# Optimization experiments

Measured on AMD Instinct MI355X. Metric: run time of the kernel, lower is better.

The kernel has to match this reference:

```python
import jax, jax.numpy as jnp
import numpy as np

TOP_K = 2
AUX_COEFF = 0.01

def setup_inputs() -> dict:
    key = jax.random.key(0)
    k1, k2, k3, k4 = jax.random.split(key, 4)
    B, T, d, E = 4, 1024, 1024, 8
    x = jax.random.normal(k1, (B, T, d), dtype=jnp.float32)
    w_gate = jax.random.normal(k2, (d, E), dtype=jnp.float32) * 0.02
    w1 = jax.random.normal(k3, (E, d, 4 * d), dtype=jnp.float32) * 0.02
    w2 = jax.random.normal(k4, (E, 4 * d, d), dtype=jnp.float32) * 0.02
    return {"x": x, "w_gate": w_gate, "w1": w1, "w2": w2}

def reference(x, w_gate, w1, w2):
    B, T, d = x.shape
    E = w_gate.shape[1]
    N = B * T
    xf = x.reshape(N, d)

    # Router: softmax over experts, top-k, renormalize
    logits = xf @ w_gate                      # [N, E]
    probs = jax.nn.softmax(logits, axis=-1)   # [N, E]
    topk_p, topk_i = jax.lax.top_k(probs, TOP_K)
    topk_p = topk_p / topk_p.sum(axis=-1, keepdims=True)

    # Combine weights: scatter top-k probs into [N, E] (equiv. to masked scatter-add loop)
    comb = jnp.zeros((N, E), dtype=x.dtype).at[
        jnp.arange(N)[:, None], topk_i].add(topk_p)

    # Grouped expert MLP (dense over experts, weighted combine)
    h = jnp.einsum('nd,edf->enf', xf, w1)     # [E, N, 4d]
    h = jax.nn.gelu(h, approximate=False)     # exact erf GELU like nn.GELU
    y = jnp.einsum('enf,efd->end', h, w2)     # [E, N, d]
    out = jnp.einsum('ne,end->nd', comb, y).reshape(B, T, d)

    # Load-balancing aux loss (training branch)
    counts = jnp.zeros((E,), dtype=x.dtype).at[topk_i.reshape(-1)].add(1.0)
    f = counts / (N * TOP_K)
    p = probs.mean(axis=0)
    aux_loss = AUX_COEFF * E * jnp.sum(f * p)
    return out, aux_loss
```

## Files before the change

### kernel.cpp

```cpp
#include <hip/hip_runtime.h>
#include <cmath>

#define N_TOK 4096
#define DDIM 1024
#define FDIM 4096
#define NEXP 8
#define MAXT 72
#define MAXROWS (MAXT * 128)

typedef __attribute__((ext_vector_type(4))) float f32x4;
typedef __attribute__((ext_vector_type(8))) __bf16 bf16x8;
typedef __attribute__((ext_vector_type(4))) unsigned short us4;
typedef __attribute__((ext_vector_type(8))) unsigned short us8;

__device__ __forceinline__ unsigned short f2bf(float f) {
  unsigned u = __builtin_bit_cast(unsigned, f);
  u += 0x7FFFu + ((u >> 16) & 1u);
  return (unsigned short)(u >> 16);
}

__device__ __forceinline__ void gload16(const void* g, void* l) {
  __builtin_amdgcn_global_load_lds(
      (const __attribute__((address_space(1))) unsigned int*)g,
      (__attribute__((address_space(3))) unsigned int*)l, 16, 0, 0);
}

__global__ __launch_bounds__(64) void router_kernel(
    const float* __restrict__ x, const float* __restrict__ wg,
    float* __restrict__ probs, int* __restrict__ eids, float* __restrict__ ewts) {
  int n = blockIdx.x;
  int t = threadIdx.x;
  const float* xr = x + (size_t)n * DDIM;
  float acc[8] = {0, 0, 0, 0, 0, 0, 0, 0};
  for (int k = t; k < DDIM; k += 64) {
    float xv = xr[k];
    const float* wr = wg + k * 8;
#pragma unroll
    for (int e = 0; e < 8; e++) acc[e] = fmaf(xv, wr[e], acc[e]);
  }
#pragma unroll
  for (int off = 32; off > 0; off >>= 1) {
#pragma unroll
    for (int e = 0; e < 8; e++) acc[e] += __shfl_xor(acc[e], off, 64);
  }
  if (t == 0) {
    float mx = acc[0];
#pragma unroll
    for (int e = 1; e < 8; e++) mx = fmaxf(mx, acc[e]);
    float p[8], s = 0.f;
#pragma unroll
    for (int e = 0; e < 8; e++) { p[e] = expf(acc[e] - mx); s += p[e]; }
    float inv = 1.f / s;
#pragma unroll
    for (int e = 0; e < 8; e++) { p[e] *= inv; probs[n * 8 + e] = p[e]; }
    int i0 = 0;
#pragma unroll
    for (int e = 1; e < 8; e++) if (p[e] > p[i0]) i0 = e;
    int i1 = (i0 == 0) ? 1 : 0;
#pragma unroll
    for (int e = 0; e < 8; e++) if (e != i0 && p[e] > p[i1]) i1 = e;
    float sw = p[i0] + p[i1];
    eids[n * 2] = i0; eids[n * 2 + 1] = i1;
    ewts[n * 2] = p[i0] / sw; ewts[n * 2 + 1] = p[i1] / sw;
  }
}

__global__ __launch_bounds__(256) void plan_kernel(
    const float* __restrict__ probs, const int* __restrict__ eids,
    float* __restrict__ aux_out, int* __restrict__ meta) {
  __shared__ float pl[256][8];
  __shared__ int cl[256][8];
  __shared__ float ps2[8];
  __shared__ int cn2[8];
  int t = threadIdx.x;
  float pa[8] = {0, 0, 0, 0, 0, 0, 0, 0};
  int ca[8] = {0, 0, 0, 0, 0, 0, 0, 0};
  for (int n = t; n < N_TOK; n += 256) {
#pragma unroll
    for (int e = 0; e < 8; e++) pa[e] += probs[n * 8 + e];
    ca[eids[n * 2]]++; ca[eids[n * 2 + 1]]++;
  }
#pragma unroll
  for (int e = 0; e < 8; e++) { pl[t][e] = pa[e]; cl[t][e] = ca[e]; }
  __syncthreads();
  if (t < 8) {
    float s = 0; int c = 0;
    for (int i = 0; i < 256; i++) { s += pl[i][t]; c += cl[i][t]; }
    ps2[t] = s; cn2[t] = c;
  }
  __syncthreads();
  if (t == 0) {
    int tb = 0; float aux = 0.f;
    for (int e = 0; e < 8; e++) {
      int c = cn2[e];
      meta[e] = c; meta[8 + e] = 0; meta[16 + e] = tb;
      int tiles = (c + 127) >> 7;
      for (int i = 0; i < tiles; i++) meta[24 + tb + i] = e;
      tb += tiles;
      aux += ((float)c / (float)(N_TOK * 2)) * (ps2[e] / (float)N_TOK);
    }
    meta[96] = tb;
    *aux_out = 0.01f * 8.f * aux;
  }
}

__global__ __launch_bounds__(256) void scatter_kernel(
    const int* __restrict__ eids, const float* __restrict__ ewts,
    int* __restrict__ meta, int* __restrict__ perm, float* __restrict__ wgt) {
  int n = blockIdx.x * 256 + threadIdx.x;
  if (n >= N_TOK) return;
#pragma unroll
  for (int s = 0; s < 2; s++) {
    int e = eids[n * 2 + s];
    int pos = atomicAdd(&meta[8 + e], 1);
    int row = (meta[16 + e] << 7) + pos;
    perm[row] = n;
    wgt[row] = ewts[n * 2 + s];
  }
}

__global__ __launch_bounds__(256) void convert_x_kernel(
    const float* __restrict__ x, unsigned short* __restrict__ xb) {
  int i = blockIdx.x * 256 + threadIdx.x;
  f32x4 v = ((const f32x4*)x)[i];
  us4 o = {f2bf(v[0]), f2bf(v[1]), f2bf(v[2]), f2bf(v[3])};
  ((us4*)xb)[i] = o;
}

__global__ __launch_bounds__(256) void transpose_conv(
    const float* __restrict__ src, unsigned short* __restrict__ dst, int R, int C) {
  __shared__ unsigned short tile[64 * 64];
  size_t eoff = (size_t)blockIdx.z * (size_t)R * (size_t)C;
  src += eoff; dst += eoff;
  int c0 = blockIdx.x << 6, r0 = blockIdx.y << 6;
  int t = threadIdx.x;
  int rl = (t >> 4) << 2;
  int cl = (t & 15) << 2;
  f32x4 v[4];
#pragma unroll
  for (int i = 0; i < 4; i++)
    v[i] = *(const f32x4*)(src + (size_t)(r0 + rl + i) * C + c0 + cl);
#pragma unroll
  for (int u = 0; u < 4; u++) {
    int c = cl + u;
    us4 o = {f2bf(v[0][u]), f2bf(v[1][u]), f2bf(v[2][u]), f2bf(v[3][u])};
    unsigned byteoff = (unsigned)c * 128 + ((((unsigned)(rl >> 3)) ^ (unsigned)(c & 7)) << 4) + (unsigned)(rl & 7) * 2;
    *(us4*)((char*)tile + byteoff) = o;
  }
  __syncthreads();
#pragma unroll
  for (int p = 0; p < 2; p++) {
    int id = t + p * 256;
    int c = id >> 3, q = id & 7;
    unsigned byteoff = (unsigned)c * 128 + (((unsigned)q ^ (unsigned)(c & 7)) << 4);
    us8 val = *(const us8*)((const char*)tile + byteoff);
    *(us8*)(dst + (size_t)(c0 + c) * R + r0 + q * 8) = val;
  }
}

template <int K, bool GATHER, int MODE>
__global__ __launch_bounds__(256, 2) void gemm_kernel(
    const unsigned short* __restrict__ A,
    const unsigned short* __restrict__ Bt,
    unsigned short* __restrict__ Hout,
    float* __restrict__ Out,
    const int* __restrict__ perm, const float* __restrict__ wgt,
    const int* __restrict__ tileExpert, const int* __restrict__ totalTiles,
    int NB) {
  __shared__ unsigned short ldsA[128 * 64];
  __shared__ unsigned short ldsB[128 * 64];
  int tile = blockIdx.x;
  if (tile >= *totalTiles) return;
  int e = tileExpert[tile];
  int m0 = tile << 7;
  int n0 = blockIdx.y << 7;
  const unsigned short* Bbase = Bt + ((size_t)e * NB + n0) * K;
  int t = threadIdx.x;
  int wave = t >> 6, lane = t & 63;
  int g = lane >> 4, ln = lane & 15;
  int wm = wave >> 1, wn = wave & 1;

  const unsigned short* srcA[4];
  const unsigned short* srcB[4];
#pragma unroll
  for (int i = 0; i < 4; i++) {
    int c = wave * 256 + i * 64 + lane;
    int r = c >> 3, kc = c & 7;
    int rowA = GATHER ? perm[m0 + r] : (m0 + r);
    srcA[i] = A + (size_t)rowA * K + ((kc ^ (r & 7)) << 3);
    srcB[i] = Bbase + (size_t)r * K + ((kc ^ (r & 7)) << 3);
  }

  f32x4 acc[4][4];
#pragma unroll
  for (int a = 0; a < 4; a++)
#pragma unroll
    for (int b = 0; b < 4; b++) acc[a][b] = (f32x4){0.f, 0.f, 0.f, 0.f};

  for (int k0 = 0; k0 < K; k0 += 64) {
#pragma unroll
    for (int i = 0; i < 4; i++) {
      int cb = wave * 256 + i * 64;
      gload16(srcA[i] + k0, &ldsA[cb * 8]);
      gload16(srcB[i] + k0, &ldsB[cb * 8]);
    }
    __syncthreads();
#pragma unroll
    for (int ks = 0; ks < 2; ks++) {
      bf16x8 af[4], bfr[4];
      int q = ks * 4 + g;
#pragma unroll
      for (int mf = 0; mf < 4; mf++) {
        int m = wm * 64 + mf * 16 + ln;
        af[mf] = *(const bf16x8*)((const char*)ldsA + m * 128 + ((q ^ (m & 7)) << 4));
      }
#pragma unroll
      for (int nf = 0; nf < 4; nf++) {
        int n = wn * 64 + nf * 16 + ln;
        bfr[nf] = *(const bf16x8*)((const char*)ldsB + n * 128 + ((q ^ (n & 7)) << 4));
      }
#pragma unroll
      for (int mf = 0; mf < 4; mf++)
#pragma unroll
        for (int nf = 0; nf < 4; nf++)
          acc[mf][nf] = __builtin_amdgcn_mfma_f32_16x16x32_bf16(af[mf], bfr[nf], acc[mf][nf], 0, 0, 0);
    }
    __syncthreads();
  }

  if (MODE == 1) {
#pragma unroll
    for (int mf = 0; mf < 4; mf++) {
#pragma unroll
      for (int r = 0; r < 4; r++) {
        int row = m0 + wm * 64 + mf * 16 + g * 4 + r;
        unsigned short* hp = Hout + (size_t)row * NB + n0 + wn * 64 + ln;
#pragma unroll
        for (int nf = 0; nf < 4; nf++) {
          float v = acc[mf][nf][r];
          v = 0.5f * v * (1.f + erff(v * 0.70710678118654752f));
          hp[nf * 16] = f2bf(v);
        }
      }
    }
  } else {
#pragma unroll
    for (int mf = 0; mf < 4; mf++) {
#pragma unroll
      for (int r = 0; r < 4; r++) {
        int prow = m0 + wm * 64 + mf * 16 + g * 4 + r;
        int token = perm[prow];
        float wv = wgt[prow];
        float* op = Out + (size_t)token * NB + n0 + wn * 64 + ln;
#pragma unroll
        for (int nf = 0; nf < 4; nf++)
          atomicAdd(op + nf * 16, wv * acc[mf][nf][r]);
      }
    }
  }
}

extern "C" void kernel_launch(void* const* d_in, const int* in_sizes, int n_in,
                              void* d_out, int out_size, void* d_ws, size_t ws_size,
                              hipStream_t stream) {
  const float* x = (const float*)d_in[0];
  const float* wgate = (const float*)d_in[1];
  const float* w1 = (const float*)d_in[2];
  const float* w2 = (const float*)d_in[3];
  float* out = (float*)d_out;

  char* w = (char*)d_ws;
  float* probs = (float*)w;                 w += (size_t)N_TOK * 8 * 4;
  int* eids = (int*)w;                      w += (size_t)N_TOK * 2 * 4;
  float* ewts = (float*)w;                  w += (size_t)N_TOK * 2 * 4;
  int* meta = (int*)w;                      w += 512;
  int* perm = (int*)w;                      w += (size_t)MAXROWS * 4;
  float* pwgt = (float*)w;                  w += (size_t)MAXROWS * 4;
  unsigned short* xb = (unsigned short*)w;  w += (size_t)N_TOK * DDIM * 2;
  unsigned short* w1t = (unsigned short*)w; w += (size_t)NEXP * DDIM * FDIM * 2;
  unsigned short* w2t = (unsigned short*)w; w += (size_t)NEXP * DDIM * FDIM * 2;
  unsigned short* h = (unsigned short*)w;   w += (size_t)MAXROWS * FDIM * 2;

  hipMemsetAsync(d_out, 0, (size_t)out_size * 4, stream);
  hipMemsetAsync(perm, 0, (size_t)MAXROWS * 8, stream);

  router_kernel<<<N_TOK, 64, 0, stream>>>(x, wgate, probs, eids, ewts);
  plan_kernel<<<1, 256, 0, stream>>>(probs, eids, out + 4194304, meta);
  scatter_kernel<<<16, 256, 0, stream>>>(eids, ewts, meta, perm, pwgt);
  convert_x_kernel<<<4096, 256, 0, stream>>>(x, xb);
  transpose_conv<<<dim3(64, 16, 8), 256, 0, stream>>>(w1, w1t, DDIM, FDIM);
  transpose_conv<<<dim3(16, 64, 8), 256, 0, stream>>>(w2, w2t, FDIM, DDIM);
  gemm_kernel<DDIM, true, 1><<<dim3(MAXT, 32), 256, 0, stream>>>(
      xb, w1t, h, nullptr, perm, pwgt, meta + 24, meta + 96, FDIM);
  gemm_kernel<FDIM, false, 2><<<dim3(MAXT, 8), 256, 0, stream>>>(
      h, w2t, nullptr, out, perm, pwgt, meta + 24, meta + 96, DDIM);
}
```

Before: 468.2 us.

## Add XCD-aware grouped tile rasterization and split-K for the down-projection GEMM

Both expert GEMMs now use a flat 1D grid. Block IDs are remapped so that consecutive logical tiles land on the same XCD, and tiles are walked in 8x8 groups of M-tiles by N-panels so blocks that share A rows and B panels run close together and reuse L2. The second GEMM (K=4096) is split into two K-slices, doubling the number of workgroups to fill more CUs; it relies on the epilogue accumulating partial results into the zeroed output. The min-occupancy hint in launch_bounds is dropped, which may change register allocation.

Result: slower. 516.8 us (+10.4%).

```diff
diff --git a/kernel.cpp b/kernel.cpp
--- a/kernel.cpp
+++ b/kernel.cpp
@@ -23,6 +23,12 @@
   __builtin_amdgcn_global_load_lds(
       (const __attribute__((address_space(1))) unsigned int*)g,
       (__attribute__((address_space(3))) unsigned int*)l, 16, 0, 0);
+}
+
+__device__ __forceinline__ int xcd_remap(int h, int nwg) {
+  int q = nwg >> 3, r = nwg & 7;
+  int xcd = h & 7, o = h >> 3;
+  return (xcd < r ? xcd * (q + 1) : r * (q + 1) + (xcd - r) * q) + o;
 }
 
 __global__ __launch_bounds__(64) void router_kernel(
@@ -158,8 +164,8 @@
   }
 }
 
-template <int K, bool GATHER, int MODE>
-__global__ __launch_bounds__(256, 2) void gemm_kernel(
+template <int K, int KSLICES, int NPANELS, bool GATHER, int MODE>
+__global__ __launch_bounds__(256) void gemm_kernel(
     const unsigned short* __restrict__ A,
     const unsigned short* __restrict__ Bt,
     unsigned short* __restrict__ Hout,
@@ -167,13 +173,24 @@
     const int* __restrict__ perm, const float* __restrict__ wgt,
     const int* __restrict__ tileExpert, const int* __restrict__ totalTiles,
     int NB) {
+  constexpr int NWG = MAXT * NPANELS * KSLICES;
+  constexpr int KB = K / KSLICES;
   __shared__ unsigned short ldsA[128 * 64];
   __shared__ unsigned short ldsB[128 * 64];
-  int tile = blockIdx.x;
-  if (tile >= *totalTiles) return;
-  int e = tileExpert[tile];
-  int m0 = tile << 7;
-  int n0 = blockIdx.y << 7;
+
+  int L = xcd_remap(blockIdx.x, NWG);
+  int group = L >> 6, wi = L & 63;
+  int gm = group % (MAXT / 8), gcol = group / (MAXT / 8);
+  int mt = gm * 8 + (wi & 7);
+  int nc = gcol * 8 + (wi >> 3);
+  int nt = nc % NPANELS;
+  int ks = nc / NPANELS;
+
+  if (mt >= *totalTiles) return;
+  int e = tileExpert[mt];
+  int m0 = mt << 7;
+  int n0 = nt << 7;
+  int k0b = ks * KB;
   const unsigned short* Bbase = Bt + ((size_t)e * NB + n0) * K;
   int t = threadIdx.x;
   int wave = t >> 6, lane = t & 63;
@@ -187,8 +204,8 @@
     int c = wave * 256 + i * 64 + lane;
     int r = c >> 3, kc = c & 7;
     int rowA = GATHER ? perm[m0 + r] : (m0 + r);
-    srcA[i] = A + (size_t)rowA * K + ((kc ^ (r & 7)) << 3);
-    srcB[i] = Bbase + (size_t)r * K + ((kc ^ (r & 7)) << 3);
+    srcA[i] = A + (size_t)rowA * K + k0b + ((kc ^ (r & 7)) << 3);
+    srcB[i] = Bbase + (size_t)r * K + k0b + ((kc ^ (r & 7)) << 3);
   }
 
   f32x4 acc[4][4];
@@ -197,7 +214,7 @@
 #pragma unroll
     for (int b = 0; b < 4; b++) acc[a][b] = (f32x4){0.f, 0.f, 0.f, 0.f};
 
-  for (int k0 = 0; k0 < K; k0 += 64) {
+  for (int k0 = 0; k0 < KB; k0 += 64) {
 #pragma unroll
     for (int i = 0; i < 4; i++) {
       int cb = wave * 256 + i * 64;
@@ -206,9 +223,9 @@
     }
     __syncthreads();
 #pragma unroll
-    for (int ks = 0; ks < 2; ks++) {
+    for (int kss = 0; kss < 2; kss++) {
       bf16x8 af[4], bfr[4];
-      int q = ks * 4 + g;
+      int q = kss * 4 + g;
 #pragma unroll
       for (int mf = 0; mf < 4; mf++) {
         int m = wm * 64 + mf * 16 + ln;
@@ -290,8 +307,8 @@
   convert_x_kernel<<<4096, 256, 0, stream>>>(x, xb);
   transpose_conv<<<dim3(64, 16, 8), 256, 0, stream>>>(w1, w1t, DDIM, FDIM);
   transpose_conv<<<dim3(16, 64, 8), 256, 0, stream>>>(w2, w2t, FDIM, DDIM);
-  gemm_kernel<DDIM, true, 1><<<dim3(MAXT, 32), 256, 0, stream>>>(
+  gemm_kernel<DDIM, 1, 32, true, 1><<<MAXT * 32, 256, 0, stream>>>(
       xb, w1t, h, nullptr, perm, pwgt, meta + 24, meta + 96, FDIM);
-  gemm_kernel<FDIM, false, 2><<<dim3(MAXT, 8), 256, 0, stream>>>(
+  gemm_kernel<FDIM, 2, 8, false, 2><<<MAXT * 16, 256, 0, stream>>>(
       h, w2t, nullptr, out, perm, pwgt, meta + 24, meta + 96, DDIM);
 }
```

## Replace atomic scatter-add in down-projection with scratch store plus combine kernel

Applied to the files above, without the earlier changes.

The second GEMM now writes plain fp32 rows into a scratch buffer that reuses the w1t workspace, which is no longer needed by then, instead of doing weighted atomicAdd into the output. A new combine kernel gathers each token's two expert rows through an inverse permutation and applies the routing weights. This removes float atomics and the output memset, at the cost of an extra round trip through scratch memory and one more launch. The padding rows in the scratch buffer get written but are never read.

New measurement: 401.9 us. 14.2% less time.

```diff
diff --git a/kernel.cpp b/kernel.cpp
--- a/kernel.cpp
+++ b/kernel.cpp
@@ -105,8 +105,8 @@
 }
 
 __global__ __launch_bounds__(256) void scatter_kernel(
-    const int* __restrict__ eids, const float* __restrict__ ewts,
-    int* __restrict__ meta, int* __restrict__ perm, float* __restrict__ wgt) {
+    const int* __restrict__ eids, int* __restrict__ meta,
+    int* __restrict__ perm, int* __restrict__ inv) {
   int n = blockIdx.x * 256 + threadIdx.x;
   if (n >= N_TOK) return;
 #pragma unroll
@@ -115,7 +115,7 @@
     int pos = atomicAdd(&meta[8 + e], 1);
     int row = (meta[16 + e] << 7) + pos;
     perm[row] = n;
-    wgt[row] = ewts[n * 2 + s];
+    inv[n * 2 + s] = row;
   }
 }
 
@@ -164,7 +164,7 @@
     const unsigned short* __restrict__ Bt,
     unsigned short* __restrict__ Hout,
     float* __restrict__ Out,
-    const int* __restrict__ perm, const float* __restrict__ wgt,
+    const int* __restrict__ perm,
     const int* __restrict__ tileExpert, const int* __restrict__ totalTiles,
     int NB) {
   __shared__ unsigned short ldsA[128 * 64];
@@ -248,16 +248,27 @@
     for (int mf = 0; mf < 4; mf++) {
 #pragma unroll
       for (int r = 0; r < 4; r++) {
-        int prow = m0 + wm * 64 + mf * 16 + g * 4 + r;
-        int token = perm[prow];
-        float wv = wgt[prow];
-        float* op = Out + (size_t)token * NB + n0 + wn * 64 + ln;
-#pragma unroll
-        for (int nf = 0; nf < 4; nf++)
-          atomicAdd(op + nf * 16, wv * acc[mf][nf][r]);
+        int row = m0 + wm * 64 + mf * 16 + g * 4 + r;
+        float* yp = Out + (size_t)row * NB + n0 + wn * 64 + ln;
+#pragma unroll
+        for (int nf = 0; nf < 4; nf++) yp[nf * 16] = acc[mf][nf][r];
       }
     }
   }
+}
+
+__global__ __launch_bounds__(256) void combine_kernel(
+    const float* __restrict__ yscr, const int* __restrict__ inv,
+    const float* __restrict__ ewts, float* __restrict__ out) {
+  int n = blockIdx.x, t = threadIdx.x;
+  int r0 = inv[n * 2], r1 = inv[n * 2 + 1];
+  float w0 = ewts[n * 2], w1 = ewts[n * 2 + 1];
+  f32x4 a = *(const f32x4*)(yscr + (size_t)r0 * DDIM + t * 4);
+  f32x4 b = *(const f32x4*)(yscr + (size_t)r1 * DDIM + t * 4);
+  f32x4 o;
+#pragma unroll
+  for (int j = 0; j < 4; j++) o[j] = w0 * a[j] + w1 * b[j];
+  *(f32x4*)(out + (size_t)n * DDIM + t * 4) = o;
 }
 
 extern "C" void kernel_launch(void* const* d_in, const int* in_sizes, int n_in,
@@ -275,23 +286,24 @@
   float* ewts = (float*)w;                  w += (size_t)N_TOK * 2 * 4;
   int* meta = (int*)w;                      w += 512;
   int* perm = (int*)w;                      w += (size_t)MAXROWS * 4;
-  float* pwgt = (float*)w;                  w += (size_t)MAXROWS * 4;
+  int* inv = (int*)w;                       w += (size_t)N_TOK * 2 * 4;
   unsigned short* xb = (unsigned short*)w;  w += (size_t)N_TOK * DDIM * 2;
   unsigned short* w1t = (unsigned short*)w; w += (size_t)NEXP * DDIM * FDIM * 2;
   unsigned short* w2t = (unsigned short*)w; w += (size_t)NEXP * DDIM * FDIM * 2;
   unsigned short* h = (unsigned short*)w;   w += (size_t)MAXROWS * FDIM * 2;
-
-  hipMemsetAsync(d_out, 0, (size_t)out_size * 4, stream);
-  hipMemsetAsync(perm, 0, (size_t)MAXROWS * 8, stream);
+  float* yscr = (float*)w1t;
+
+  hipMemsetAsync(perm, 0, (size_t)MAXROWS * 4, stream);
 
   router_kernel<<<N_TOK, 64, 0, stream>>>(x, wgate, probs, eids, ewts);
   plan_kernel<<<1, 256, 0, stream>>>(probs, eids, out + 4194304, meta);
-  scatter_kernel<<<16, 256, 0, stream>>>(eids, ewts, meta, perm, pwgt);
+  scatter_kernel<<<16, 256, 0, stream>>>(eids, meta, perm, inv);
   convert_x_kernel<<<4096, 256, 0, stream>>>(x, xb);
   transpose_conv<<<dim3(64, 16, 8), 256, 0, stream>>>(w1, w1t, DDIM, FDIM);
   transpose_conv<<<dim3(16, 64, 8), 256, 0, stream>>>(w2, w2t, FDIM, DDIM);
   gemm_kernel<DDIM, true, 1><<<dim3(MAXT, 32), 256, 0, stream>>>(
-      xb, w1t, h, nullptr, perm, pwgt, meta + 24, meta + 96, FDIM);
+      xb, w1t, h, nullptr, perm, meta + 24, meta + 96, FDIM);
   gemm_kernel<FDIM, false, 2><<<dim3(MAXT, 8), 256, 0, stream>>>(
-      h, w2t, nullptr, out, perm, pwgt, meta + 24, meta + 96, DDIM);
-}
+      h, w2t, nullptr, yscr, perm, meta + 24, meta + 96, DDIM);
+  combine_kernel<<<N_TOK, 256, 0, stream>>>(yscr, inv, ewts, out);
+}
```
